# Kernel optimization log

Hardware: AMD Instinct MI355X
Metric: run time of the kernel (lower is better)

## Reference

```python
import jax, jax.numpy as jnp
import numpy as np
import math

D_MODEL = 1024
NUM_HEADS = 16
D_K = D_MODEL // NUM_HEADS
SEQ_LEN = 2048
THETA = 10000.0


def _rope_tables(seq_len, d_k, theta):
    # inv_freq over even dims, angles repeated-interleaved to full d_k
    inv_freq = theta ** (-jnp.arange(0, d_k, 2, dtype=jnp.float32) / d_k)  # [d_k/2]
    pos = jnp.arange(seq_len, dtype=jnp.float32)                          # [s]
    angles = pos[:, None] * inv_freq[None, :]                             # [s, d_k/2]
    angles = jnp.repeat(angles, 2, axis=-1)                               # [s, d_k]
    return jnp.cos(angles), jnp.sin(angles)


def _rotate_half(x):
    # interleaved pairs: (x0,x1,x2,x3,...) -> (-x1,x0,-x3,x2,...)
    x_even = x[..., ::2]
    x_odd = x[..., 1::2]
    return jnp.stack([-x_odd, x_even], axis=-1).reshape(x.shape)


def _apply_rope(x, cos, sin):
    # x: [b, h, s, d_k]; cos/sin: [s, d_k]
    return x * cos + _rotate_half(x) * sin


def setup_inputs() -> dict:
    key = jax.random.key(0)
    ks = jax.random.split(key, 5)
    scale = 1.0 / math.sqrt(D_MODEL)
    X = jax.random.normal(ks[0], (2, SEQ_LEN, D_MODEL), dtype=jnp.float32)
    Wq = jax.random.normal(ks[1], (D_MODEL, D_MODEL), dtype=jnp.float32) * scale
    Wk = jax.random.normal(ks[2], (D_MODEL, D_MODEL), dtype=jnp.float32) * scale
    Wv = jax.random.normal(ks[3], (D_MODEL, D_MODEL), dtype=jnp.float32) * scale
    Wo = jax.random.normal(ks[4], (D_MODEL, D_MODEL), dtype=jnp.float32) * scale
    return {"X": X, "Wq": Wq, "Wk": Wk, "Wv": Wv, "Wo": Wo}


def reference(X, Wq, Wk, Wv, Wo):
    b, s, _ = X.shape
    h, dk = NUM_HEADS, D_K

    def proj(W):
        return (X @ W.T).reshape(b, s, h, dk).transpose(0, 2, 1, 3)  # [b,h,s,dk]

    q, k, v = proj(Wq), proj(Wk), proj(Wv)

    cos, sin = _rope_tables(s, dk, THETA)
    q = _apply_rope(q, cos, sin)
    k = _apply_rope(k, cos, sin)

    scores = jnp.einsum('bhid,bhjd->bhij', q, k) / math.sqrt(dk)
    causal = jnp.tril(jnp.ones((s, s), dtype=bool))
    scores = jnp.where(causal[None, None], scores, -jnp.inf)
    probs = jax.nn.softmax(scores, axis=-1)
    attended = jnp.einsum('bhij,bhjd->bhid', probs, v)               # [b,h,s,dk]

    out = attended.transpose(0, 2, 1, 3).reshape(b, s, h * dk)
    return out @ Wo.T
```

## Files before the change

### kernel.cpp

```cpp
#include <hip/hip_runtime.h>
#include <stdint.h>

#define D_MODEL 1024
#define NUM_HEADS 16
#define DK 64
#define SEQ 2048
#define BATCH 2
#define MROWS (BATCH * SEQ)
#define LOG2E 1.4426950408889634f
#define FIXM 14.0f

typedef short bf16x8 __attribute__((ext_vector_type(8)));
typedef float f32x4 __attribute__((ext_vector_type(4)));

__device__ __forceinline__ unsigned short f2bf(float f) {
    unsigned int u = __float_as_uint(f);
    u = (u + 0x7fffu + ((u >> 16) & 1u)) >> 16;
    return (unsigned short)u;
}
__device__ __forceinline__ unsigned short f2bf_trunc(float f) {
    return (unsigned short)(__float_as_uint(f) >> 16);
}
__device__ __forceinline__ float bf2f(unsigned short h) {
    return __uint_as_float(((unsigned int)h) << 16);
}
__device__ __forceinline__ void async16(const void* g, void* l) {
    __builtin_amdgcn_global_load_lds(
        (const __attribute__((address_space(1))) void*)g,
        (__attribute__((address_space(3))) void*)l, 16, 0, 0);
}
#define SWZ64(row, b) ((((row) * 8) + ((b) ^ ((row) & 7))) * 8)

__global__ void cast_all(const float4* __restrict__ X, const float4* __restrict__ Wq,
                         const float4* __restrict__ Wk, const float4* __restrict__ Wv,
                         const float4* __restrict__ Wo, ushort4* __restrict__ Xb,
                         ushort4* __restrict__ Wqkvb, ushort4* __restrict__ Wob) {
    int i = blockIdx.x * blockDim.x + threadIdx.x;
    const float4* src;
    ushort4* dst;
    int off;
    if (i < 1048576) { src = X; dst = Xb; off = i; }
    else if (i < 1310720) { src = Wq; dst = Wqkvb; off = i - 1048576; }
    else if (i < 1572864) { src = Wk; dst = Wqkvb + 262144; off = i - 1310720; }
    else if (i < 1835008) { src = Wv; dst = Wqkvb + 524288; off = i - 1572864; }
    else { src = Wo; dst = Wob; off = i - 1835008; }
    float4 v = src[off];
    ushort4 o;
    o.x = f2bf(v.x); o.y = f2bf(v.y); o.z = f2bf(v.z); o.w = f2bf(v.w);
    dst[off] = o;
}

template <int OUT_BF16>
__global__ __launch_bounds__(256) void gemm128(
    const unsigned short* __restrict__ A, const unsigned short* __restrict__ B,
    void* __restrict__ Cout, int M, int N, int K) {
    __shared__ unsigned short As[128 * 64];
    __shared__ unsigned short Bs[128 * 64];
    const int m0 = blockIdx.y * 128, n0 = blockIdx.x * 128;
    const int t = threadIdx.x;
    const int lane = t & 63, wave = t >> 6;
    const int mA = lane & 15, quad = lane >> 4;
    const int wr = (wave >> 1) * 64, wc = (wave & 1) * 64;

    f32x4 acc[4][4] = {};
    for (int k0 = 0; k0 < K; k0 += 64) {
#pragma unroll
        for (int i = 0; i < 4; ++i) {
            int ch = i * 256 + t;
            int r = ch >> 3, bsw = ch & 7;
            int b = bsw ^ (r & 7);
            async16(A + (size_t)(m0 + r) * K + k0 + b * 8, (char*)As + ch * 16);
            async16(B + (size_t)(n0 + r) * K + k0 + b * 8, (char*)Bs + ch * 16);
        }
        __syncthreads();
#pragma unroll
        for (int kk = 0; kk < 2; ++kk) {
            bf16x8 af[4], bfr[4];
#pragma unroll
            for (int mi = 0; mi < 4; ++mi) {
                int rr = wr + mi * 16 + mA;
                af[mi] = *(const bf16x8*)&As[SWZ64(rr, kk * 4 + quad)];
            }
#pragma unroll
            for (int ni = 0; ni < 4; ++ni) {
                int rr = wc + ni * 16 + mA;
                bfr[ni] = *(const bf16x8*)&Bs[SWZ64(rr, kk * 4 + quad)];
            }
#pragma unroll
            for (int mi = 0; mi < 4; ++mi)
#pragma unroll
                for (int ni = 0; ni < 4; ++ni)
                    acc[mi][ni] = __builtin_amdgcn_mfma_f32_16x16x32_bf16(
                        af[mi], bfr[ni], acc[mi][ni], 0, 0, 0);
        }
        __syncthreads();
    }
#pragma unroll
    for (int mi = 0; mi < 4; ++mi)
#pragma unroll
        for (int ni = 0; ni < 4; ++ni)
#pragma unroll
            for (int r = 0; r < 4; ++r) {
                int gm = m0 + wr + mi * 16 + quad * 4 + r;
                int gn = n0 + wc + ni * 16 + mA;
                if (OUT_BF16)
                    ((unsigned short*)Cout)[(size_t)gm * N + gn] = f2bf(acc[mi][ni][r]);
                else
                    ((float*)Cout)[(size_t)gm * N + gn] = acc[mi][ni][r];
            }
}

__global__ void rope_qk(const unsigned short* __restrict__ QKV,
                        unsigned short* __restrict__ Qr,
                        unsigned short* __restrict__ Kr) {
    int tid = blockIdx.x * blockDim.x + threadIdx.x;
    int bs = tid >> 8;
    int p4 = tid & 255;
    int b = bs >> 11, spos = bs & 2047;
    int h = p4 >> 4, dd = (p4 & 15) * 4;

    float sn0, cs0, sn1, cs1;
    {
        float if0 = __expf(-(float)dd * (9.210340371976184f / 64.0f));
        float if1 = __expf(-(float)(dd + 2) * (9.210340371976184f / 64.0f));
        __sincosf((float)spos * if0, &sn0, &cs0);
        __sincosf((float)spos * if1, &sn1, &cs1);
    }
    size_t src = (size_t)bs * 3072 + h * 64 + dd;
    ushort4 qw = *(const ushort4*)&QKV[src];
    ushort4 kw = *(const ushort4*)&QKV[src + 1024];

    ushort4 qo_, ko_;
    {
        float e = bf2f(qw.x), o = bf2f(qw.y);
        qo_.x = f2bf(e * cs0 - o * sn0); qo_.y = f2bf(o * cs0 + e * sn0);
        e = bf2f(qw.z); o = bf2f(qw.w);
        qo_.z = f2bf(e * cs1 - o * sn1); qo_.w = f2bf(o * cs1 + e * sn1);
        e = bf2f(kw.x); o = bf2f(kw.y);
        ko_.x = f2bf(e * cs0 - o * sn0); ko_.y = f2bf(o * cs0 + e * sn0);
        e = bf2f(kw.z); o = bf2f(kw.w);
        ko_.z = f2bf(e * cs1 - o * sn1); ko_.w = f2bf(o * cs1 + e * sn1);
    }
    size_t qb = (((size_t)(b * NUM_HEADS + h) * SEQ + spos) * DK + dd);
    *(ushort4*)&Qr[qb] = qo_;
    *(ushort4*)&Kr[qb] = ko_;
}

__global__ __launch_bounds__(256) void vtrans(const unsigned short* __restrict__ QKV,
                                              unsigned short* __restrict__ Vt) {
    __shared__ unsigned short T[64][80];
    const int bh = blockIdx.y, s0 = blockIdx.x * 64;
    const int b = bh >> 4, h = bh & 15;
    const int t = threadIdx.x;
#pragma unroll
    for (int i = 0; i < 2; ++i) {
        int ch = i * 256 + t;
        int row = ch >> 3, bc = ch & 7;
        *(int4*)&T[row][bc * 8] =
            *(const int4*)&QKV[(size_t)(b * SEQ + s0 + row) * 3072 + 2048 + h * 64 + bc * 8];
    }
    __syncthreads();
#pragma unroll
    for (int i = 0; i < 2; ++i) {
        int ch = i * 256 + t;
        int d = ch >> 3, sb = ch & 7;
        unsigned short tmp[8];
#pragma unroll
        for (int j = 0; j < 8; ++j) tmp[j] = T[sb * 8 + j][d];
        *(int4*)&Vt[(size_t)bh * DK * SEQ + (size_t)d * SEQ + s0 + sb * 8] = *(int4*)tmp;
    }
}

__global__ __launch_bounds__(256) void flash_attn5(
    const unsigned short* __restrict__ Qr, const unsigned short* __restrict__ Kr,
    const unsigned short* __restrict__ Vt, unsigned short* __restrict__ Att) {
    __shared__ unsigned short Ks[2][64 * 64];
    __shared__ unsigned short Vs[2][64 * 64];
    __shared__ unsigned short Ps[4][16 * 72];
    __shared__ float Lw[2][4][16];
    const int bh = blockIdx.y;
    const int tp = blockIdx.x;
    const int ta = tp, tb = 31 - tp;
    const int t = threadIdx.x;
    const int lane = t & 63, wave = t >> 6;
    const int mA = lane & 15, quad = lane >> 4;
    const int qr0a = ta * 64 + wave * 16;
    const int qr0b = tb * 64 + wave * 16;
    const size_t qkbase = (size_t)bh * SEQ * DK;
    const unsigned short* Kg = Kr + qkbase;
    const unsigned short* Vg = Vt + (size_t)bh * DK * SEQ;

    bf16x8 aqa[2], aqb[2];
#pragma unroll
    for (int c = 0; c < 2; ++c) {
        bf16x8 ra = *(const bf16x8*)&Qr[qkbase + (size_t)(qr0a + mA) * DK + c * 32 + quad * 8];
        bf16x8 rb = *(const bf16x8*)&Qr[qkbase + (size_t)(qr0b + mA) * DK + c * 32 + quad * 8];
        bf16x8 sa, sb2;
#pragma unroll
        for (int j = 0; j < 8; ++j) {
            sa[j] = (short)f2bf(bf2f((unsigned short)ra[j]) * (0.125f * LOG2E));
            sb2[j] = (short)f2bf(bf2f((unsigned short)rb[j]) * (0.125f * LOG2E));
        }
        aqa[c] = sa; aqb[c] = sb2;
    }

    f32x4 accA[4] = {}, accB[4] = {};
    float lsumA[4] = {}, lsumB[4] = {};

#pragma unroll
    for (int i = 0; i < 2; ++i) {
        int ch = i * 256 + t;
        int row = ch >> 3, sb = (ch & 7) ^ (row & 7);
        async16(Kg + (size_t)row * DK + sb * 8, (char*)Ks[0] + ch * 16);
        async16(Vg + (size_t)row * SEQ + sb * 8, (char*)Vs[0] + ch * 16);
    }

    for (int jt = 0; jt <= tb; ++jt) {
        __syncthreads();
        const int cur = jt & 1;
        if (jt < tb) {
            const int j1 = (jt + 1) * 64;
#pragma unroll
            for (int i = 0; i < 2; ++i) {
                int ch = i * 256 + t;
                int row = ch >> 3, sb = (ch & 7) ^ (row & 7);
                async16(Kg + (size_t)(j1 + row) * DK + sb * 8, (char*)Ks[cur ^ 1] + ch * 16);
                async16(Vg + (size_t)row * SEQ + j1 + sb * 8, (char*)Vs[cur ^ 1] + ch * 16);
            }
        }
        const int j0 = jt * 64;
        const unsigned short* Kt = Ks[cur];
        const unsigned short* Vtile = Vs[cur];
        unsigned short* Pw = Ps[wave];

#pragma unroll
        for (int side = 0; side < 2; ++side) {
            if (side == 1 && jt > ta) break;
            const bf16x8* aq = side ? aqa : aqb;
            f32x4* accT = side ? accA : accB;
            float* lsum = side ? lsumA : lsumB;
            const int qr0 = side ? qr0a : qr0b;
            const int myqt = side ? ta : tb;

            f32x4 sc[4] = {};
#pragma unroll
            for (int js = 0; js < 4; ++js) {
                int row = js * 16 + mA;
                bf16x8 b0 = *(const bf16x8*)&Kt[SWZ64(row, quad)];
                bf16x8 b1 = *(const bf16x8*)&Kt[SWZ64(row, quad + 4)];
                sc[js] = __builtin_amdgcn_mfma_f32_16x16x32_bf16(aq[0], b0, sc[js], 0, 0, 0);
                sc[js] = __builtin_amdgcn_mfma_f32_16x16x32_bf16(aq[1], b1, sc[js], 0, 0, 0);
            }
            if (jt == myqt) {
#pragma unroll
                for (int js = 0; js < 4; ++js) {
                    int gcol = j0 + js * 16 + mA;
#pragma unroll
                    for (int r = 0; r < 4; ++r)
                        if (gcol > qr0 + quad * 4 + r) sc[js][r] = -1e30f;
                }
            }
#pragma unroll
            for (int js = 0; js < 4; ++js)
#pragma unroll
                for (int r = 0; r < 4; ++r) {
                    float p = __builtin_amdgcn_exp2f(sc[js][r] - FIXM);
                    lsum[r] += p;
                    Pw[(quad * 4 + r) * 72 + js * 16 + mA] = f2bf_trunc(p);
                }
            bf16x8 ap0 = *(const bf16x8*)&Pw[mA * 72 + quad * 8];
            bf16x8 ap1 = *(const bf16x8*)&Pw[mA * 72 + 32 + quad * 8];
#pragma unroll
            for (int tn = 0; tn < 4; ++tn) {
                int row = tn * 16 + mA;
                bf16x8 bv0 = *(const bf16x8*)&Vtile[SWZ64(row, quad)];
                bf16x8 bv1 = *(const bf16x8*)&Vtile[SWZ64(row, quad + 4)];
                accT[tn] = __builtin_amdgcn_mfma_f32_16x16x32_bf16(bv0, ap0, accT[tn], 0, 0, 0);
                accT[tn] = __builtin_amdgcn_mfma_f32_16x16x32_bf16(bv1, ap1, accT[tn], 0, 0, 0);
            }
        }
    }

#pragma unroll
    for (int r = 0; r < 4; ++r) {
#pragma unroll
        for (int off = 1; off < 16; off <<= 1) {
            lsumA[r] += __shfl_xor(lsumA[r], off, 64);
            lsumB[r] += __shfl_xor(lsumB[r], off, 64);
        }
    }
    if (mA == 0)
#pragma unroll
        for (int r = 0; r < 4; ++r) {
            Lw[0][wave][quad * 4 + r] = lsumA[r];
            Lw[1][wave][quad * 4 + r] = lsumB[r];
        }
    __syncthreads();
    const float rlA = 1.0f / Lw[0][wave][mA];
    const float rlB = 1.0f / Lw[1][wave][mA];

    const int b = bh >> 4, h = bh & 15;
#pragma unroll
    for (int tn = 0; tn < 4; ++tn) {
        ushort4 oa, ob;
        oa.x = f2bf(accA[tn][0] * rlA); oa.y = f2bf(accA[tn][1] * rlA);
        oa.z = f2bf(accA[tn][2] * rlA); oa.w = f2bf(accA[tn][3] * rlA);
        ob.x = f2bf(accB[tn][0] * rlB); ob.y = f2bf(accB[tn][1] * rlB);
        ob.z = f2bf(accB[tn][2] * rlB); ob.w = f2bf(accB[tn][3] * rlB);
        *(ushort4*)&Att[(size_t)(b * SEQ + qr0a + mA) * D_MODEL + h * DK + tn * 16 + quad * 4] = oa;
        *(ushort4*)&Att[(size_t)(b * SEQ + qr0b + mA) * D_MODEL + h * DK + tn * 16 + quad * 4] = ob;
    }
}

extern "C" void kernel_launch(void* const* d_in, const int* in_sizes, int n_in,
                              void* d_out, int out_size, void* d_ws, size_t ws_size,
                              hipStream_t stream) {
    const float* X = (const float*)d_in[0];
    const float* Wq = (const float*)d_in[1];
    const float* Wk = (const float*)d_in[2];
    const float* Wv = (const float*)d_in[3];
    const float* Wo = (const float*)d_in[4];

    char* ws = (char*)d_ws;
    unsigned short* Xb     = (unsigned short*)(ws + 0);
    unsigned short* Wqkvb  = (unsigned short*)(ws + (8u << 20));
    unsigned short* Wob    = (unsigned short*)(ws + (14u << 20));
    unsigned short* QKVraw = (unsigned short*)(ws + (16u << 20));
    unsigned short* Kr     = (unsigned short*)(ws + (40u << 20));
    unsigned short* Vt     = (unsigned short*)(ws + (48u << 20));
    unsigned short* Qr     = Xb;
    unsigned short* Att    = QKVraw;

    cast_all<<<8192, 256, 0, stream>>>((const float4*)X, (const float4*)Wq,
                                       (const float4*)Wk, (const float4*)Wv,
                                       (const float4*)Wo, (ushort4*)Xb,
                                       (ushort4*)Wqkvb, (ushort4*)Wob);

    gemm128<1><<<dim3(3072 / 128, MROWS / 128), 256, 0, stream>>>(
        Xb, Wqkvb, QKVraw, MROWS, 3072, D_MODEL);

    rope_qk<<<(MROWS * 256) / 256, 256, 0, stream>>>(QKVraw, Qr, Kr);
    vtrans<<<dim3(SEQ / 64, BATCH * NUM_HEADS), 256, 0, stream>>>(QKVraw, Vt);

    flash_attn5<<<dim3(16, BATCH * NUM_HEADS), 256, 0, stream>>>(Qr, Kr, Vt, Att);

    gemm128<0><<<dim3(D_MODEL / 128, MROWS / 128), 256, 0, stream>>>(
        Att, Wob, d_out, MROWS, D_MODEL, D_MODEL);
}
```

Measured before the change: 196.8 us.

## Split attention to one query tile per block, merge rope/vtrans, narrower out-proj tiles

Flash attention now gives each block a single query tile (grid 32x32, longest tiles first) instead of pairing tiles ta and 31-ta. It also adds launch_bounds occupancy 4, swizzles the P scratch and reuses Ks for the row sums. The rope and V-transpose kernels are merged into one launch, and the output projection uses 128x64 tiles to launch twice as many blocks. The aim is more parallelism and fewer launches, at the cost of losing the paired-tile load balancing and of smaller GEMM tiles with less reuse.

Result: faster. 182.1 us (-7.5%).

```diff
diff --git a/kernel.cpp b/kernel.cpp
--- a/kernel.cpp
+++ b/kernel.cpp
@@ -50,55 +50,62 @@
     dst[off] = o;
 }
 
-template <int OUT_BF16>
-__global__ __launch_bounds__(256) void gemm128(
+template <int TN, int OUT_BF16>
+__global__ __launch_bounds__(256) void gemm_tile(
     const unsigned short* __restrict__ A, const unsigned short* __restrict__ B,
     void* __restrict__ Cout, int M, int N, int K) {
     __shared__ unsigned short As[128 * 64];
-    __shared__ unsigned short Bs[128 * 64];
-    const int m0 = blockIdx.y * 128, n0 = blockIdx.x * 128;
+    __shared__ unsigned short Bs[TN * 64];
+    const int m0 = blockIdx.y * 128, n0 = blockIdx.x * TN;
     const int t = threadIdx.x;
     const int lane = t & 63, wave = t >> 6;
     const int mA = lane & 15, quad = lane >> 4;
-    const int wr = (wave >> 1) * 64, wc = (wave & 1) * 64;
-
-    f32x4 acc[4][4] = {};
+    constexpr int MI = (TN == 128) ? 4 : 2;
+    constexpr int NI = 4;
+    const int wr = (TN == 128) ? (wave >> 1) * 64 : wave * 32;
+    const int wc = (TN == 128) ? (wave & 1) * 64 : 0;
+
+    f32x4 acc[MI][NI] = {};
     for (int k0 = 0; k0 < K; k0 += 64) {
 #pragma unroll
         for (int i = 0; i < 4; ++i) {
             int ch = i * 256 + t;
-            int r = ch >> 3, bsw = ch & 7;
-            int b = bsw ^ (r & 7);
+            int r = ch >> 3, b = (ch & 7) ^ (r & 7);
             async16(A + (size_t)(m0 + r) * K + k0 + b * 8, (char*)As + ch * 16);
+        }
+#pragma unroll
+        for (int i = 0; i < TN / 32; ++i) {
+            int ch = i * 256 + t;
+            int r = ch >> 3, b = (ch & 7) ^ (r & 7);
             async16(B + (size_t)(n0 + r) * K + k0 + b * 8, (char*)Bs + ch * 16);
         }
         __syncthreads();
 #pragma unroll
         for (int kk = 0; kk < 2; ++kk) {
-            bf16x8 af[4], bfr[4];
-#pragma unroll
-            for (int mi = 0; mi < 4; ++mi) {
+            bf16x8 af[MI], bfr[NI];
+#pragma unroll
+            for (int mi = 0; mi < MI; ++mi) {
                 int rr = wr + mi * 16 + mA;
                 af[mi] = *(const bf16x8*)&As[SWZ64(rr, kk * 4 + quad)];
             }
 #pragma unroll
-            for (int ni = 0; ni < 4; ++ni) {
+            for (int ni = 0; ni < NI; ++ni) {
                 int rr = wc + ni * 16 + mA;
                 bfr[ni] = *(const bf16x8*)&Bs[SWZ64(rr, kk * 4 + quad)];
             }
 #pragma unroll
-            for (int mi = 0; mi < 4; ++mi)
-#pragma unroll
-                for (int ni = 0; ni < 4; ++ni)
+            for (int mi = 0; mi < MI; ++mi)
+#pragma unroll
+                for (int ni = 0; ni < NI; ++ni)
                     acc[mi][ni] = __builtin_amdgcn_mfma_f32_16x16x32_bf16(
                         af[mi], bfr[ni], acc[mi][ni], 0, 0, 0);
         }
         __syncthreads();
     }
 #pragma unroll
-    for (int mi = 0; mi < 4; ++mi)
-#pragma unroll
-        for (int ni = 0; ni < 4; ++ni)
+    for (int mi = 0; mi < MI; ++mi)
+#pragma unroll
+        for (int ni = 0; ni < NI; ++ni)
 #pragma unroll
             for (int r = 0; r < 4; ++r) {
                 int gm = m0 + wr + mi * 16 + quad * 4 + r;
@@ -110,28 +117,30 @@
             }
 }
 
-__global__ void rope_qk(const unsigned short* __restrict__ QKV,
-                        unsigned short* __restrict__ Qr,
-                        unsigned short* __restrict__ Kr) {
-    int tid = blockIdx.x * blockDim.x + threadIdx.x;
-    int bs = tid >> 8;
-    int p4 = tid & 255;
-    int b = bs >> 11, spos = bs & 2047;
-    int h = p4 >> 4, dd = (p4 & 15) * 4;
-
-    float sn0, cs0, sn1, cs1;
-    {
-        float if0 = __expf(-(float)dd * (9.210340371976184f / 64.0f));
-        float if1 = __expf(-(float)(dd + 2) * (9.210340371976184f / 64.0f));
-        __sincosf((float)spos * if0, &sn0, &cs0);
-        __sincosf((float)spos * if1, &sn1, &cs1);
-    }
-    size_t src = (size_t)bs * 3072 + h * 64 + dd;
-    ushort4 qw = *(const ushort4*)&QKV[src];
-    ushort4 kw = *(const ushort4*)&QKV[src + 1024];
-
-    ushort4 qo_, ko_;
-    {
+__global__ __launch_bounds__(256) void rope_vt(const unsigned short* __restrict__ QKV,
+                                               unsigned short* __restrict__ Qr,
+                                               unsigned short* __restrict__ Kr,
+                                               unsigned short* __restrict__ Vt) {
+    __shared__ unsigned short T[64][80];
+    const int bx = blockIdx.x;
+    const int t = threadIdx.x;
+    if (bx < 4096) {
+        int tid = bx * 256 + t;
+        int bs = tid >> 8;
+        int p4 = tid & 255;
+        int b = bs >> 11, spos = bs & 2047;
+        int h = p4 >> 4, dd = (p4 & 15) * 4;
+        float sn0, cs0, sn1, cs1;
+        {
+            float if0 = __expf(-(float)dd * (9.210340371976184f / 64.0f));
+            float if1 = __expf(-(float)(dd + 2) * (9.210340371976184f / 64.0f));
+            __sincosf((float)spos * if0, &sn0, &cs0);
+            __sincosf((float)spos * if1, &sn1, &cs1);
+        }
+        size_t src = (size_t)bs * 3072 + h * 64 + dd;
+        ushort4 qw = *(const ushort4*)&QKV[src];
+        ushort4 kw = *(const ushort4*)&QKV[src + 1024];
+        ushort4 qo_, ko_;
         float e = bf2f(qw.x), o = bf2f(qw.y);
         qo_.x = f2bf(e * cs0 - o * sn0); qo_.y = f2bf(o * cs0 + e * sn0);
         e = bf2f(qw.z); o = bf2f(qw.w);
@@ -140,72 +149,62 @@
         ko_.x = f2bf(e * cs0 - o * sn0); ko_.y = f2bf(o * cs0 + e * sn0);
         e = bf2f(kw.z); o = bf2f(kw.w);
         ko_.z = f2bf(e * cs1 - o * sn1); ko_.w = f2bf(o * cs1 + e * sn1);
-    }
-    size_t qb = (((size_t)(b * NUM_HEADS + h) * SEQ + spos) * DK + dd);
-    *(ushort4*)&Qr[qb] = qo_;
-    *(ushort4*)&Kr[qb] = ko_;
-}
-
-__global__ __launch_bounds__(256) void vtrans(const unsigned short* __restrict__ QKV,
-                                              unsigned short* __restrict__ Vt) {
-    __shared__ unsigned short T[64][80];
-    const int bh = blockIdx.y, s0 = blockIdx.x * 64;
-    const int b = bh >> 4, h = bh & 15;
-    const int t = threadIdx.x;
-#pragma unroll
-    for (int i = 0; i < 2; ++i) {
-        int ch = i * 256 + t;
-        int row = ch >> 3, bc = ch & 7;
-        *(int4*)&T[row][bc * 8] =
-            *(const int4*)&QKV[(size_t)(b * SEQ + s0 + row) * 3072 + 2048 + h * 64 + bc * 8];
-    }
-    __syncthreads();
-#pragma unroll
-    for (int i = 0; i < 2; ++i) {
-        int ch = i * 256 + t;
-        int d = ch >> 3, sb = ch & 7;
-        unsigned short tmp[8];
-#pragma unroll
-        for (int j = 0; j < 8; ++j) tmp[j] = T[sb * 8 + j][d];
-        *(int4*)&Vt[(size_t)bh * DK * SEQ + (size_t)d * SEQ + s0 + sb * 8] = *(int4*)tmp;
-    }
-}
-
-__global__ __launch_bounds__(256) void flash_attn5(
+        size_t qb = (((size_t)(b * NUM_HEADS + h) * SEQ + spos) * DK + dd);
+        *(ushort4*)&Qr[qb] = qo_;
+        *(ushort4*)&Kr[qb] = ko_;
+    } else {
+        int idx = bx - 4096;
+        const int s0 = (idx & 31) * 64, bh = idx >> 5;
+        const int b = bh >> 4, h = bh & 15;
+#pragma unroll
+        for (int i = 0; i < 2; ++i) {
+            int ch = i * 256 + t;
+            int row = ch >> 3, bc = ch & 7;
+            *(int4*)&T[row][bc * 8] =
+                *(const int4*)&QKV[(size_t)(b * SEQ + s0 + row) * 3072 + 2048 + h * 64 + bc * 8];
+        }
+        __syncthreads();
+#pragma unroll
+        for (int i = 0; i < 2; ++i) {
+            int ch = i * 256 + t;
+            int d = ch >> 3, sb = ch & 7;
+            unsigned short tmp[8];
+#pragma unroll
+            for (int j = 0; j < 8; ++j) tmp[j] = T[sb * 8 + j][d];
+            *(int4*)&Vt[(size_t)bh * DK * SEQ + (size_t)d * SEQ + s0 + sb * 8] = *(int4*)tmp;
+        }
+    }
+}
+
+__global__ __launch_bounds__(256, 4) void flash_attn6(
     const unsigned short* __restrict__ Qr, const unsigned short* __restrict__ Kr,
     const unsigned short* __restrict__ Vt, unsigned short* __restrict__ Att) {
     __shared__ unsigned short Ks[2][64 * 64];
     __shared__ unsigned short Vs[2][64 * 64];
-    __shared__ unsigned short Ps[4][16 * 72];
-    __shared__ float Lw[2][4][16];
-    const int bh = blockIdx.y;
-    const int tp = blockIdx.x;
-    const int ta = tp, tb = 31 - tp;
+    __shared__ unsigned short Ps[4][16 * 64];
+    const int bh = blockIdx.x;
+    const int qt = 31 - (int)blockIdx.y;
     const int t = threadIdx.x;
     const int lane = t & 63, wave = t >> 6;
     const int mA = lane & 15, quad = lane >> 4;
-    const int qr0a = ta * 64 + wave * 16;
-    const int qr0b = tb * 64 + wave * 16;
+    const int qr0 = qt * 64 + wave * 16;
     const size_t qkbase = (size_t)bh * SEQ * DK;
     const unsigned short* Kg = Kr + qkbase;
     const unsigned short* Vg = Vt + (size_t)bh * DK * SEQ;
 
-    bf16x8 aqa[2], aqb[2];
+    bf16x8 aq[2];
 #pragma unroll
     for (int c = 0; c < 2; ++c) {
-        bf16x8 ra = *(const bf16x8*)&Qr[qkbase + (size_t)(qr0a + mA) * DK + c * 32 + quad * 8];
-        bf16x8 rb = *(const bf16x8*)&Qr[qkbase + (size_t)(qr0b + mA) * DK + c * 32 + quad * 8];
-        bf16x8 sa, sb2;
-#pragma unroll
-        for (int j = 0; j < 8; ++j) {
-            sa[j] = (short)f2bf(bf2f((unsigned short)ra[j]) * (0.125f * LOG2E));
-            sb2[j] = (short)f2bf(bf2f((unsigned short)rb[j]) * (0.125f * LOG2E));
-        }
-        aqa[c] = sa; aqb[c] = sb2;
-    }
-
-    f32x4 accA[4] = {}, accB[4] = {};
-    float lsumA[4] = {}, lsumB[4] = {};
+        bf16x8 raw = *(const bf16x8*)&Qr[qkbase + (size_t)(qr0 + mA) * DK + c * 32 + quad * 8];
+        bf16x8 s;
+#pragma unroll
+        for (int j = 0; j < 8; ++j)
+            s[j] = (short)f2bf(bf2f((unsigned short)raw[j]) * (0.125f * LOG2E));
+        aq[c] = s;
+    }
+
+    f32x4 accT[4] = {};
+    float lsum[4] = {};
 
 #pragma unroll
     for (int i = 0; i < 2; ++i) {
@@ -215,10 +214,10 @@
         async16(Vg + (size_t)row * SEQ + sb * 8, (char*)Vs[0] + ch * 16);
     }
 
-    for (int jt = 0; jt <= tb; ++jt) {
+    for (int jt = 0; jt <= qt; ++jt) {
         __syncthreads();
         const int cur = jt & 1;
-        if (jt < tb) {
+        if (jt < qt) {
             const int j1 = (jt + 1) * 64;
 #pragma unroll
             for (int i = 0; i < 2; ++i) {
@@ -233,82 +232,68 @@
         const unsigned short* Vtile = Vs[cur];
         unsigned short* Pw = Ps[wave];
 
-#pragma unroll
-        for (int side = 0; side < 2; ++side) {
-            if (side == 1 && jt > ta) break;
-            const bf16x8* aq = side ? aqa : aqb;
-            f32x4* accT = side ? accA : accB;
-            float* lsum = side ? lsumA : lsumB;
-            const int qr0 = side ? qr0a : qr0b;
-            const int myqt = side ? ta : tb;
-
-            f32x4 sc[4] = {};
+        f32x4 sc[4] = {};
+#pragma unroll
+        for (int js = 0; js < 4; ++js) {
+            int row = js * 16 + mA;
+            bf16x8 b0 = *(const bf16x8*)&Kt[SWZ64(row, quad)];
+            bf16x8 b1 = *(const bf16x8*)&Kt[SWZ64(row, quad + 4)];
+            sc[js] = __builtin_amdgcn_mfma_f32_16x16x32_bf16(aq[0], b0, sc[js], 0, 0, 0);
+            sc[js] = __builtin_amdgcn_mfma_f32_16x16x32_bf16(aq[1], b1, sc[js], 0, 0, 0);
+        }
+        if (jt == qt) {
 #pragma unroll
             for (int js = 0; js < 4; ++js) {
-                int row = js * 16 + mA;
-                bf16x8 b0 = *(const bf16x8*)&Kt[SWZ64(row, quad)];
-                bf16x8 b1 = *(const bf16x8*)&Kt[SWZ64(row, quad + 4)];
-                sc[js] = __builtin_amdgcn_mfma_f32_16x16x32_bf16(aq[0], b0, sc[js], 0, 0, 0);
-                sc[js] = __builtin_amdgcn_mfma_f32_16x16x32_bf16(aq[1], b1, sc[js], 0, 0, 0);
-            }
-            if (jt == myqt) {
-#pragma unroll
-                for (int js = 0; js < 4; ++js) {
-                    int gcol = j0 + js * 16 + mA;
-#pragma unroll
-                    for (int r = 0; r < 4; ++r)
-                        if (gcol > qr0 + quad * 4 + r) sc[js][r] = -1e30f;
-                }
-            }
-#pragma unroll
-            for (int js = 0; js < 4; ++js)
-#pragma unroll
-                for (int r = 0; r < 4; ++r) {
-                    float p = __builtin_amdgcn_exp2f(sc[js][r] - FIXM);
-                    lsum[r] += p;
-                    Pw[(quad * 4 + r) * 72 + js * 16 + mA] = f2bf_trunc(p);
-                }
-            bf16x8 ap0 = *(const bf16x8*)&Pw[mA * 72 + quad * 8];
-            bf16x8 ap1 = *(const bf16x8*)&Pw[mA * 72 + 32 + quad * 8];
-#pragma unroll
-            for (int tn = 0; tn < 4; ++tn) {
-                int row = tn * 16 + mA;
-                bf16x8 bv0 = *(const bf16x8*)&Vtile[SWZ64(row, quad)];
-                bf16x8 bv1 = *(const bf16x8*)&Vtile[SWZ64(row, quad + 4)];
-                accT[tn] = __builtin_amdgcn_mfma_f32_16x16x32_bf16(bv0, ap0, accT[tn], 0, 0, 0);
-                accT[tn] = __builtin_amdgcn_mfma_f32_16x16x32_bf16(bv1, ap1, accT[tn], 0, 0, 0);
-            }
-        }
-    }
-
-#pragma unroll
-    for (int r = 0; r < 4; ++r) {
-#pragma unroll
-        for (int off = 1; off < 16; off <<= 1) {
-            lsumA[r] += __shfl_xor(lsumA[r], off, 64);
-            lsumB[r] += __shfl_xor(lsumB[r], off, 64);
-        }
-    }
+                int gcol = j0 + js * 16 + mA;
+#pragma unroll
+                for (int r = 0; r < 4; ++r)
+                    if (gcol > qr0 + quad * 4 + r) sc[js][r] = -1e30f;
+            }
+        }
+
+#pragma unroll
+        for (int js = 0; js < 4; ++js)
+#pragma unroll
+            for (int r = 0; r < 4; ++r) {
+                float p = __builtin_amdgcn_exp2f(sc[js][r] - FIXM);
+                lsum[r] += p;
+                int q = quad * 4 + r;
+                Pw[SWZ64(q, js * 2 + (mA >> 3)) + (mA & 7)] = f2bf_trunc(p);
+            }
+        bf16x8 ap0 = *(const bf16x8*)&Pw[SWZ64(mA, quad)];
+        bf16x8 ap1 = *(const bf16x8*)&Pw[SWZ64(mA, quad + 4)];
+#pragma unroll
+        for (int tn = 0; tn < 4; ++tn) {
+            int row = tn * 16 + mA;
+            bf16x8 bv0 = *(const bf16x8*)&Vtile[SWZ64(row, quad)];
+            bf16x8 bv1 = *(const bf16x8*)&Vtile[SWZ64(row, quad + 4)];
+            accT[tn] = __builtin_amdgcn_mfma_f32_16x16x32_bf16(bv0, ap0, accT[tn], 0, 0, 0);
+            accT[tn] = __builtin_amdgcn_mfma_f32_16x16x32_bf16(bv1, ap1, accT[tn], 0, 0, 0);
+        }
+    }
+
+#pragma unroll
+    for (int r = 0; r < 4; ++r)
+#pragma unroll
+        for (int off = 1; off < 16; off <<= 1)
+            lsum[r] += __shfl_xor(lsum[r], off, 64);
+    __syncthreads();
+    float* LL = (float*)Ks;
     if (mA == 0)
 #pragma unroll
-        for (int r = 0; r < 4; ++r) {
-            Lw[0][wave][quad * 4 + r] = lsumA[r];
-            Lw[1][wave][quad * 4 + r] = lsumB[r];
-        }
+        for (int r = 0; r < 4; ++r) LL[wave * 16 + quad * 4 + r] = lsum[r];
     __syncthreads();
-    const float rlA = 1.0f / Lw[0][wave][mA];
-    const float rlB = 1.0f / Lw[1][wave][mA];
+    const float rl = 1.0f / LL[wave * 16 + mA];
 
     const int b = bh >> 4, h = bh & 15;
 #pragma unroll
     for (int tn = 0; tn < 4; ++tn) {
-        ushort4 oa, ob;
-        oa.x = f2bf(accA[tn][0] * rlA); oa.y = f2bf(accA[tn][1] * rlA);
-        oa.z = f2bf(accA[tn][2] * rlA); oa.w = f2bf(accA[tn][3] * rlA);
-        ob.x = f2bf(accB[tn][0] * rlB); ob.y = f2bf(accB[tn][1] * rlB);
-        ob.z = f2bf(accB[tn][2] * rlB); ob.w = f2bf(accB[tn][3] * rlB);
-        *(ushort4*)&Att[(size_t)(b * SEQ + qr0a + mA) * D_MODEL + h * DK + tn * 16 + quad * 4] = oa;
-        *(ushort4*)&Att[(size_t)(b * SEQ + qr0b + mA) * D_MODEL + h * DK + tn * 16 + quad * 4] = ob;
+        ushort4 o;
+        o.x = f2bf(accT[tn][0] * rl);
+        o.y = f2bf(accT[tn][1] * rl);
+        o.z = f2bf(accT[tn][2] * rl);
+        o.w = f2bf(accT[tn][3] * rl);
+        *(ushort4*)&Att[(size_t)(b * SEQ + qr0 + mA) * D_MODEL + h * DK + tn * 16 + quad * 4] = o;
     }
 }
 
@@ -336,14 +321,13 @@
                                        (const float4*)Wo, (ushort4*)Xb,
                                        (ushort4*)Wqkvb, (ushort4*)Wob);
 
-    gemm128<1><<<dim3(3072 / 128, MROWS / 128), 256, 0, stream>>>(
+    gemm_tile<128, 1><<<dim3(3072 / 128, MROWS / 128), 256, 0, stream>>>(
         Xb, Wqkvb, QKVraw, MROWS, 3072, D_MODEL);
 
-    rope_qk<<<(MROWS * 256) / 256, 256, 0, stream>>>(QKVraw, Qr, Kr);
-    vtrans<<<dim3(SEQ / 64, BATCH * NUM_HEADS), 256, 0, stream>>>(QKVraw, Vt);
-
-    flash_attn5<<<dim3(16, BATCH * NUM_HEADS), 256, 0, stream>>>(Qr, Kr, Vt, Att);
-
-    gemm128<0><<<dim3(D_MODEL / 128, MROWS / 128), 256, 0, stream>>>(
+    rope_vt<<<4096 + 1024, 256, 0, stream>>>(QKVraw, Qr, Kr, Vt);
+
+    flash_attn6<<<dim3(BATCH * NUM_HEADS, 32), 256, 0, stream>>>(Qr, Kr, Vt, Att);
+
+    gemm_tile<64, 0><<<dim3(D_MODEL / 64, MROWS / 128), 256, 0, stream>>>(
         Att, Wob, d_out, MROWS, D_MODEL, D_MODEL);
 }
```
